# Performance work log

Hardware: AMD Instinct MI355X
Metric: run time of the kernel (lower is better)

The kernel has to match this reference:

```python
import jax, jax.numpy as jnp
import numpy as np

B, SQ, SV = 2, 2048, 2048
DV, DQ, DK, DO, H = 1024, 1280, 1024, 1024, 16
DHK, DHO = DK // H, DO // H


def setup_inputs() -> dict:
    key = jax.random.key(0)
    ks = jax.random.split(key, 8)
    pre_value_key = jax.random.normal(ks[0], (B, SV, DV), jnp.float32)
    pre_query = jax.random.normal(ks[1], (B, SQ, DQ), jnp.float32)
    value_key_masks = (jax.random.uniform(ks[2], (B, SV)) < 0.9).astype(jnp.float32)
    value_key_counts = jnp.maximum(value_key_masks.sum(-1), 1.0)
    s = 0.02
    Wq = jax.random.normal(ks[3], (DQ, DK), jnp.float32) * s
    bq = jnp.zeros((DK,), jnp.float32)
    Wk = jax.random.normal(ks[4], (DV, DK), jnp.float32) * s
    bk = jnp.zeros((DK,), jnp.float32)
    Wv = jax.random.normal(ks[5], (DV, DO), jnp.float32) * s
    bv = jnp.zeros((DO,), jnp.float32)
    overall_gain = jnp.ones((1, H, 1, 1), jnp.float32)
    overall_bias = jnp.full((1, H, 1, 1), -10.0, jnp.float32)
    return dict(pre_value_key=pre_value_key, pre_query=pre_query,
                value_key_masks=value_key_masks, value_key_counts=value_key_counts,
                Wq=Wq, bq=bq, Wk=Wk, bk=bk, Wv=Wv, bv=bv,
                overall_gain=overall_gain, overall_bias=overall_bias)


def _heads(x, h):
    # (B, S, D) -> (B, h, S, D//h)
    b, s, d = x.shape
    return x.reshape(b, s, h, d // h).transpose(0, 2, 1, 3)


def reference(pre_value_key, pre_query, value_key_masks, value_key_counts,
              Wq, bq, Wk, bk, Wv, bv, overall_gain, overall_bias):
    q = _heads(pre_query @ Wq + bq, H)        # (B,H,SQ,DHK)
    k = _heads(pre_value_key @ Wk + bk, H)    # (B,H,SV,DHK)
    v = _heads(pre_value_key @ Wv + bv, H)    # (B,H,SV,DHO)

    scores = jnp.einsum('bhqd,bhkd->bhqk', q, k) / jnp.sqrt(jnp.float32(DHK))

    mask = value_key_masks  # (B,SV), 0/1 float
    # pooled-score sigmoid gate (cross-attn branch)
    pooled = (scores * mask[:, None, None, :]).sum(-1, keepdims=True)
    pooled = pooled / value_key_counts[:, None, None, None]
    overall_weight = jax.nn.sigmoid(pooled * overall_gain + overall_bias)  # (B,H,SQ,1)

    add_mask = jnp.where(mask == 0, -jnp.inf, 0.0).astype(scores.dtype)
    sm = jax.nn.softmax(scores + add_mask[:, None, None, :], axis=-1)
    h = jnp.einsum('bhqk,bhkd->bhqd', sm, v)  # (B,H,SQ,DHO)

    pq_split = _heads(pre_query[:, :, :DO], H)  # (B,H,SQ,DHO)
    out = pq_split * (1.0 - overall_weight) + h * overall_weight
    out = out.transpose(0, 2, 1, 3).reshape(B, SQ, DO)
    out = jnp.concatenate([out, pre_query[:, :, DO:]], axis=-1)  # (B,SQ,DQ)
    return out
```

## Files before the change

### kernel.cpp

```cpp
#include <hip/hip_runtime.h>

typedef __attribute__((ext_vector_type(8))) __bf16 bf16x8;
typedef __attribute__((ext_vector_type(4))) float f32x4;
typedef __attribute__((ext_vector_type(16))) float f32x16;
typedef __attribute__((ext_vector_type(4))) unsigned short us4;
typedef __attribute__((ext_vector_type(4))) unsigned int u32x4;
typedef __attribute__((ext_vector_type(2))) unsigned int u32x2;
typedef __attribute__((address_space(3))) void* as3vp;
typedef const __attribute__((address_space(1))) void* as1vp;

#define GLOAD_LDS16(g, l) __builtin_amdgcn_global_load_lds((as1vp)(g), (as3vp)(l), 16, 0, 0)

#if __has_builtin(__builtin_amdgcn_exp2f)
#define EXP2(x) __builtin_amdgcn_exp2f(x)
#else
#define EXP2(x) __expf((x) * 0.6931471805599453f)
#endif

__device__ __forceinline__ unsigned short f2bf(float f) {
  unsigned u = __builtin_bit_cast(unsigned, f);
  u += 0x7FFFu + ((u >> 16) & 1u);
  return (unsigned short)(u >> 16);
}
__device__ __forceinline__ float bf2f(unsigned short u) {
  return __builtin_bit_cast(float, (unsigned)u << 16);
}
__device__ __forceinline__ unsigned int pkbf(float a, float b) {
  unsigned int r;
  asm("v_cvt_pk_bf16_f32 %0, %1, %2" : "=v"(r) : "v"(a), "v"(b));
  return r;
}

__global__ void cvt_pq_tail(const float* __restrict__ x, unsigned short* __restrict__ y,
                            float* __restrict__ out) {
  const int i = blockIdx.x * 256 + threadIdx.x;
  if (i >= 1310720) return;
  float4 v = ((const float4*)x)[i];
  us4 o;
  o.x = f2bf(v.x); o.y = f2bf(v.y); o.z = f2bf(v.z); o.w = f2bf(v.w);
  ((us4*)y)[i] = o;
  if ((i % 320) >= 256) ((float4*)out)[i] = v;
}

__global__ void cvt_f32_bf16(const float* __restrict__ x, unsigned short* __restrict__ y, int n4) {
  int i = blockIdx.x * 256 + threadIdx.x;
  if (i >= n4) return;
  float4 v = ((const float4*)x)[i];
  us4 o;
  o.x = f2bf(v.x); o.y = f2bf(v.y); o.z = f2bf(v.z); o.w = f2bf(v.w);
  ((us4*)y)[i] = o;
}

__global__ void transpose_w3(const float* __restrict__ Wq, const float* __restrict__ Wk,
                             const float* __restrict__ Wv,
                             unsigned short* __restrict__ WqT, unsigned short* __restrict__ WkT,
                             unsigned short* __restrict__ WvT) {
  const int z = blockIdx.z;
  const int K = (z == 0) ? 1280 : 1024;
  if ((int)blockIdx.y * 32 >= K) return;
  const float* W = (z == 0) ? Wq : ((z == 1) ? Wk : Wv);
  unsigned short* WT = (z == 0) ? WqT : ((z == 1) ? WkT : WvT);
  __shared__ float t[32][33];
  const int tx = threadIdx.x & 31, ty = threadIdx.x >> 5;
  const int n0 = blockIdx.x * 32, k0 = blockIdx.y * 32;
#pragma unroll
  for (int i = 0; i < 32; i += 8)
    t[ty + i][tx] = W[(size_t)(k0 + ty + i) * 1024 + n0 + tx];
  __syncthreads();
#pragma unroll
  for (int i = 0; i < 32; i += 8)
    WT[(size_t)(n0 + ty + i) * K + k0 + tx] = f2bf(t[tx][ty + i]);
}

__global__ void km_reduce(const unsigned short* __restrict__ Kbb, const float* __restrict__ mask,
                          float* __restrict__ km, float* __restrict__ addm) {
  if (blockIdx.x < 16) {
    const int i = blockIdx.x * 256 + threadIdx.x;
    addm[i] = (mask[i] != 0.f) ? 0.f : -1e30f;
  }
  __shared__ float red[16][64];
  const int bh = blockIdx.x >> 3, chunk = blockIdx.x & 7;
  const int b = bh >> 4;
  const int dg = (threadIdx.x & 15) * 4, rg = threadIdx.x >> 4;
  const unsigned short* kb = Kbb + (size_t)(b * 2048) * 1024 + (bh & 15) * 64 + dg;
  const float* mr = mask + b * 2048;
  float a0 = 0.f, a1 = 0.f, a2 = 0.f, a3 = 0.f;
  const int kv0 = chunk * 256;
#pragma unroll 4
  for (int kv = kv0 + rg; kv < kv0 + 256; kv += 16) {
    const float mv = mr[kv];
    us4 kq = *(const us4*)(kb + (size_t)kv * 1024);
    a0 = fmaf(mv, bf2f(kq.x), a0); a1 = fmaf(mv, bf2f(kq.y), a1);
    a2 = fmaf(mv, bf2f(kq.z), a2); a3 = fmaf(mv, bf2f(kq.w), a3);
  }
  red[rg][dg] = a0; red[rg][dg + 1] = a1; red[rg][dg + 2] = a2; red[rg][dg + 3] = a3;
  __syncthreads();
  if (threadIdx.x < 64) {
    float s = 0.f;
#pragma unroll
    for (int i = 0; i < 16; ++i) s += red[i][threadIdx.x];
    atomicAdd(&km[bh * 64 + threadIdx.x], s);
  }
}

__global__ __launch_bounds__(256, 2)
void gemm_all(const unsigned short* __restrict__ Aq,
              const unsigned short* __restrict__ Akv,
              const unsigned short* __restrict__ WqT,
              const unsigned short* __restrict__ WkT,
              const unsigned short* __restrict__ WvT,
              const float* __restrict__ bq,
              const float* __restrict__ bk,
              const float* __restrict__ bv,
              unsigned short* __restrict__ Qout,
              unsigned short* __restrict__ Kout,
              unsigned short* __restrict__ VFout) {
  __shared__ unsigned short sA[2][128 * 64];
  __shared__ unsigned short sB[2][128 * 64];
  const int z = blockIdx.z;
  const int KDIM = (z == 0) ? 1280 : 1024;
  const unsigned short* A = (z == 0) ? Aq : Akv;
  const unsigned short* Bt = (z == 0) ? WqT : ((z == 1) ? WkT : WvT);

  const int tid = threadIdx.x, lane = tid & 63, w = tid >> 6;
  const int l15 = lane & 15, lhi = lane >> 4;
  const int wm = w >> 1, wn = w & 1;
  const int row0 = blockIdx.x * 128, col0 = blockIdx.y * 128;

  const f32x4 zv = {0.f, 0.f, 0.f, 0.f};
  f32x4 acc[4][4];
#pragma unroll
  for (int m = 0; m < 4; ++m)
#pragma unroll
    for (int n = 0; n < 4; ++n) acc[m][n] = zv;

  auto stage = [&](int buf, int kt) {
#pragma unroll
    for (int i = 0; i < 4; ++i) {
      const int c = i * 256 + tid;
      const int r = c >> 3, kc = ((c & 7) ^ (r & 7)) * 8;
      GLOAD_LDS16(A + (size_t)(row0 + r) * KDIM + kt + kc, &sA[buf][0] + c * 8);
      GLOAD_LDS16(Bt + (size_t)(col0 + r) * KDIM + kt + kc, &sB[buf][0] + c * 8);
    }
  };

  const int NT = KDIM / 64;
  stage(0, 0);
  __syncthreads();
  int cur = 0;
  for (int t = 0; t < NT; ++t) {
    if (t + 1 < NT) stage(cur ^ 1, (t + 1) * 64);
    const unsigned short* sAb = &sA[cur][0];
    const unsigned short* sBb = &sB[cur][0];
#pragma unroll
    for (int ks = 0; ks < 2; ++ks) {
      const int koS = (ks * 32 + lhi * 8) ^ ((l15 & 7) * 8);
      bf16x8 af[4], bfr[4];
#pragma unroll
      for (int m = 0; m < 4; ++m) af[m] = *(const bf16x8*)(sAb + (wm * 64 + m * 16 + l15) * 64 + koS);
#pragma unroll
      for (int n = 0; n < 4; ++n) bfr[n] = *(const bf16x8*)(sBb + (wn * 64 + n * 16 + l15) * 64 + koS);
#pragma unroll
      for (int m = 0; m < 4; ++m)
#pragma unroll
        for (int n = 0; n < 4; ++n)
          acc[m][n] = __builtin_amdgcn_mfma_f32_16x16x32_bf16(af[m], bfr[n], acc[m][n], 0, 0, 0);
    }
    __syncthreads();
    cur ^= 1;
  }

  if (z <= 1) {
    unsigned short* C = (z == 0) ? Qout : Kout;
    const float* bias = (z == 0) ? bq : bk;
    const float scale = (z == 0) ? 0.18033688f : 1.0f;
#pragma unroll
    for (int n = 0; n < 4; ++n) {
      const int gc = col0 + wn * 64 + n * 16 + l15;
      const float bb = bias[gc];
#pragma unroll
      for (int m = 0; m < 4; ++m) {
        const int gr0 = row0 + wm * 64 + m * 16 + lhi * 4;
#pragma unroll
        for (int r = 0; r < 4; ++r)
          C[(size_t)(gr0 + r) * 1024 + gc] = f2bf((acc[m][n][r] + bb) * scale);
      }
    }
  } else {
    __syncthreads();
    unsigned* tb = (unsigned*)&sA[0][0];
#pragma unroll
    for (int n = 0; n < 4; ++n) {
      const int gcL = wn * 64 + n * 16 + l15;
      const float bb = bv[col0 + gcL];
#pragma unroll
      for (int m = 0; m < 4; ++m) {
#pragma unroll
        for (int k = 0; k < 2; ++k) {
          const int grPair = wm * 32 + m * 8 + lhi * 2 + k;
          const int W = (grPair & 3) | ((((grPair >> 2) ^ gcL) & 15) << 2);
          tb[gcL * 64 + W] = pkbf(acc[m][n][2 * k] + bb, acc[m][n][2 * k + 1] + bb);
        }
      }
    }
    __syncthreads();
    const int b_ = row0 >> 11;
#pragma unroll
    for (int it = 0; it < 8; ++it) {
      const int c = it * 256 + tid;
      const int gcL = (c & 63) + ((c >> 10) << 6);
      const int u = (c >> 6) & 15;
      const int W4 = (u ^ gcL) & 15;
      u32x4 o = *(const u32x4*)(tb + gcL * 64 + W4 * 4);
      const int kv0 = (row0 & 2047) + u * 8;
      const int ch = col0 + gcL;
      const int hh2 = ch >> 6, d = ch & 63;
      const int t2 = kv0 >> 6, ks2 = (kv0 >> 4) & 3, h5v = (kv0 >> 3) & 1;
      const size_t off = ((size_t)(b_ * 16 + hh2) << 17) +
                         (size_t)(((t2 * 4 + ks2) * 2 + (d >> 5)) * 64 + h5v * 32 + (d & 31)) * 8;
      *(u32x4*)(VFout + off) = o;
    }
  }
}

__global__ __launch_bounds__(256, 2)
void attn_fused(const unsigned short* __restrict__ Q,
                const unsigned short* __restrict__ Kb,
                const unsigned short* __restrict__ VF,
                const float* __restrict__ addm_g,
                const float* __restrict__ km,
                const float* __restrict__ counts,
                const float* __restrict__ gain,
                const float* __restrict__ gbias,
                const float* __restrict__ pq,
                float* __restrict__ out) {
  __shared__ __align__(16) char smem[32768];
  unsigned short* sK = (unsigned short*)smem;
  float* saddm = (float*)(smem + 16384);
  float* sOT = (float*)smem;

  const int tid = threadIdx.x, lane = tid & 63, w = tid >> 6;
  const int l31 = lane & 31, h5 = lane >> 5;
  const int f = blockIdx.x;
  const int qt = (f >> 3) & 15;
  const int bh = (f & 7) + 8 * (f >> 7);
  const int b = bh >> 4, hh = bh & 15;
  const int q0 = qt * 128;

  GLOAD_LDS16(addm_g + b * 2048 + tid * 4, (char*)saddm + tid * 16);
  GLOAD_LDS16(addm_g + b * 2048 + 1024 + tid * 4, (char*)saddm + 4096 + tid * 16);

  bf16x8 qf[4];
  {
    const unsigned short* qp = Q + (size_t)(b * 2048 + q0 + w * 32 + l31) * 1024 + hh * 64 + h5 * 8;
#pragma unroll
    for (int ks = 0; ks < 4; ++ks) qf[ks] = *(const bf16x8*)(qp + ks * 16);
  }

  float pl_s = 0.f;
  {
    const float* kmp = km + (b * 16 + hh) * 64 + h5 * 8;
#pragma unroll
    for (int ks = 0; ks < 4; ++ks) {
      f32x4 ka = *(const f32x4*)(kmp + ks * 16);
      f32x4 kb4 = *(const f32x4*)(kmp + ks * 16 + 4);
#pragma unroll
      for (int j = 0; j < 4; ++j)
        pl_s += (float)qf[ks][j] * ka[j] + (float)qf[ks][j + 4] * kb4[j];
    }
    float ta = pl_s, tb = pl_s;
    asm("v_permlane32_swap_b32 %0, %1" : "+v"(ta), "+v"(tb));
    pl_s = ta + tb;
  }

  const unsigned short* Kbase = Kb + (size_t)(b * 2048) * 1024 + hh * 64;
  const unsigned short* VFb = VF + ((size_t)bh << 17) + lane * 8;

  f32x16 o0, o1, l_vec;
#pragma unroll
  for (int r = 0; r < 16; ++r) { o0[r] = 0.f; o1[r] = 0.f; l_vec[r] = 0.f; }
  float m_ = -1e30f;

  auto stageK = [&](int buf, int kv) {
#pragma unroll
    for (int i = 0; i < 2; ++i) {
      const int c = i * 256 + tid;
      const int r = c >> 3, sl = (c & 7) ^ (r & 7);
      GLOAD_LDS16(Kbase + (size_t)(kv + r) * 1024 + sl * 8, (char*)sK + buf * 8192 + c * 16);
    }
  };

  bf16x8 vf[8];
  auto ldV = [&](int t) {
    const unsigned short* p = VFb + (size_t)t * 4096;
#pragma unroll
    for (int i = 0; i < 8; ++i) vf[i] = *(const bf16x8*)(p + i * 512);
  };

  stageK(0, 0);
  __syncthreads();
  int cur = 0;

  for (int t = 0; t < 32; ++t) {
    if (t < 31) stageK(cur ^ 1, (t + 1) * 64);
    ldV(t);
    const char* sKc = (const char*)sK + cur * 8192;

    f32x16 s0, s1;
#pragma unroll
    for (int g = 0; g < 4; ++g) {
      f32x4 a0 = *(const f32x4*)(saddm + t * 64 + g * 8 + h5 * 4);
      f32x4 a1 = *(const f32x4*)(saddm + t * 64 + 32 + g * 8 + h5 * 4);
#pragma unroll
      for (int j = 0; j < 4; ++j) { s0[g * 4 + j] = a0[j]; s1[g * 4 + j] = a1[j]; }
    }

#pragma unroll
    for (int ks = 0; ks < 4; ++ks) {
      const int sl = (((ks * 2 + h5) ^ (l31 & 7)) * 16);
      bf16x8 k0 = *(const bf16x8*)(sKc + l31 * 128 + sl);
      bf16x8 k1 = *(const bf16x8*)(sKc + (32 + l31) * 128 + sl);
      s0 = __builtin_amdgcn_mfma_f32_32x32x16_bf16(k0, qf[ks], s0, 0, 0, 0);
      s1 = __builtin_amdgcn_mfma_f32_32x32x16_bf16(k1, qf[ks], s1, 0, 0, 0);
    }

    f32x16 mx;
#pragma unroll
    for (int r = 0; r < 16; ++r) mx[r] = fmaxf(s0[r], s1[r]);
    float t8[8];
#pragma unroll
    for (int r = 0; r < 8; ++r) t8[r] = fmaxf(mx[r], mx[r + 8]);
    float tp = fmaxf(fmaxf(fmaxf(t8[0], t8[1]), fmaxf(t8[2], t8[3])),
                     fmaxf(fmaxf(t8[4], t8[5]), fmaxf(t8[6], t8[7])));
    {
      float ta = tp, tb = tp;
      asm("v_permlane32_swap_b32 %0, %1" : "+v"(ta), "+v"(tb));
      tp = fmaxf(ta, tb);
    }
    if (__any(tp > m_ + 11.0f)) {
      const float mnew = fmaxf(m_, tp);
      const float corr = EXP2(m_ - mnew);
      m_ = mnew;
      l_vec *= corr; o0 *= corr; o1 *= corr;
    }

    f32x16 p0, p1;
#pragma unroll
    for (int r = 0; r < 16; ++r) p0[r] = EXP2(s0[r] - m_);
#pragma unroll
    for (int r = 0; r < 16; ++r) p1[r] = EXP2(s1[r] - m_);
    l_vec += p0; l_vec += p1;

    bf16x8 pfs[4];
    {
      unsigned x0 = pkbf(p0[0], p0[1]), y0 = pkbf(p0[2], p0[3]);
      unsigned z0 = pkbf(p0[4], p0[5]), w0 = pkbf(p0[6], p0[7]);
      asm("v_permlane32_swap_b32 %0, %1" : "+v"(x0), "+v"(z0));
      asm("v_permlane32_swap_b32 %0, %1" : "+v"(y0), "+v"(w0));
      u32x4 f0 = {x0, y0, z0, w0};
      pfs[0] = __builtin_bit_cast(bf16x8, f0);
      unsigned x1 = pkbf(p0[8], p0[9]), y1 = pkbf(p0[10], p0[11]);
      unsigned z1 = pkbf(p0[12], p0[13]), w1 = pkbf(p0[14], p0[15]);
      asm("v_permlane32_swap_b32 %0, %1" : "+v"(x1), "+v"(z1));
      asm("v_permlane32_swap_b32 %0, %1" : "+v"(y1), "+v"(w1));
      u32x4 f1 = {x1, y1, z1, w1};
      pfs[1] = __builtin_bit_cast(bf16x8, f1);
      unsigned x2 = pkbf(p1[0], p1[1]), y2 = pkbf(p1[2], p1[3]);
      unsigned z2 = pkbf(p1[4], p1[5]), w2 = pkbf(p1[6], p1[7]);
      asm("v_permlane32_swap_b32 %0, %1" : "+v"(x2), "+v"(z2));
      asm("v_permlane32_swap_b32 %0, %1" : "+v"(y2), "+v"(w2));
      u32x4 f2 = {x2, y2, z2, w2};
      pfs[2] = __builtin_bit_cast(bf16x8, f2);
      unsigned x3 = pkbf(p1[8], p1[9]), y3 = pkbf(p1[10], p1[11]);
      unsigned z3 = pkbf(p1[12], p1[13]), w3 = pkbf(p1[14], p1[15]);
      asm("v_permlane32_swap_b32 %0, %1" : "+v"(x3), "+v"(z3));
      asm("v_permlane32_swap_b32 %0, %1" : "+v"(y3), "+v"(w3));
      u32x4 f3 = {x3, y3, z3, w3};
      pfs[3] = __builtin_bit_cast(bf16x8, f3);
    }

#pragma unroll
    for (int ks = 0; ks < 4; ++ks) {
      o0 = __builtin_amdgcn_mfma_f32_32x32x16_bf16(vf[ks * 2], pfs[ks], o0, 0, 0, 0);
      o1 = __builtin_amdgcn_mfma_f32_32x32x16_bf16(vf[ks * 2 + 1], pfs[ks], o1, 0, 0, 0);
    }
    __syncthreads();
    cur ^= 1;
  }

  float l_s;
  {
    float a[8];
#pragma unroll
    for (int r = 0; r < 8; ++r) a[r] = l_vec[r] + l_vec[r + 8];
    l_s = ((a[0] + a[1]) + (a[2] + a[3])) + ((a[4] + a[5]) + (a[6] + a[7]));
    float ta = l_s, tb = l_s;
    asm("v_permlane32_swap_b32 %0, %1" : "+v"(ta), "+v"(tb));
    l_s = ta + tb;
  }
  const float po = pl_s * 0.6931471805599453f / counts[b];
  const float wgv = 1.f / (1.f + __expf(-(po * gain[hh] + gbias[hh])));
  const float invl = 1.f / l_s;

  __syncthreads();
  float* myOT = sOT + w * 2048;
#pragma unroll
  for (int r = 0; r < 16; ++r) {
    const int d0 = (r & 3) + 8 * (r >> 2) + 4 * h5;
    myOT[d0 * 32 + (l31 ^ (d0 & 31))] = o0[r] * invl;
    const int d1 = d0 + 32;
    myOT[d1 * 32 + (l31 ^ (d1 & 31))] = o1[r] * invl;
  }
  __syncthreads();
  const size_t rowbase = (size_t)(b * 2048 + q0 + w * 32) * 1280 + hh * 64 + lane;
  const float* pqrow = pq + rowbase;
  float* outrow = out + rowbase;
#pragma unroll 4
  for (int i = 0; i < 32; ++i) {
    const float hval = myOT[lane * 32 + (i ^ (lane & 31))];
    const float wgrow = __shfl(wgv, i, 64);
    const float pv = pqrow[(size_t)i * 1280];
    outrow[(size_t)i * 1280] = fmaf(hval - pv, wgrow, pv);
  }
}

extern "C" void kernel_launch(void* const* d_in, const int* in_sizes, int n_in,
                              void* d_out, int out_size, void* d_ws, size_t ws_size,
                              hipStream_t stream) {
  const float* pre_vk = (const float*)d_in[0];
  const float* pre_q  = (const float*)d_in[1];
  const float* vmask  = (const float*)d_in[2];
  const float* vcnt   = (const float*)d_in[3];
  const float* Wq = (const float*)d_in[4];
  const float* bq = (const float*)d_in[5];
  const float* Wk = (const float*)d_in[6];
  const float* bk = (const float*)d_in[7];
  const float* Wv = (const float*)d_in[8];
  const float* bv = (const float*)d_in[9];
  const float* gain  = (const float*)d_in[10];
  const float* gbias = (const float*)d_in[11];
  float* out = (float*)d_out;

  char* ws = (char*)d_ws;
  unsigned short* pq_bf = (unsigned short*)(ws);
  unsigned short* pv_bf = (unsigned short*)(ws + 10485760);
  unsigned short* WqT   = (unsigned short*)(ws + 18874368);
  unsigned short* WkT   = (unsigned short*)(ws + 21495808);
  unsigned short* WvT   = (unsigned short*)(ws + 23592960);
  unsigned short* Qb    = (unsigned short*)(ws + 25690112);
  unsigned short* Kbb   = (unsigned short*)(ws + 34078720);
  unsigned short* VFb   = (unsigned short*)(ws + 42467328);
  float*          kmb   = (float*)(ws + 50855936);
  float*          addm  = (float*)(ws + 50864128);

  hipMemsetAsync(kmb, 0, 2 * 16 * 64 * sizeof(float), stream);
  cvt_pq_tail<<<5120, 256, 0, stream>>>(pre_q, pq_bf, out);
  cvt_f32_bf16<<<4096, 256, 0, stream>>>(pre_vk, pv_bf, 1048576);
  transpose_w3<<<dim3(32, 40, 3), 256, 0, stream>>>(Wq, Wk, Wv, WqT, WkT, WvT);
  gemm_all<<<dim3(32, 8, 3), 256, 0, stream>>>(pq_bf, pv_bf, WqT, WkT, WvT, bq, bk, bv, Qb, Kbb, VFb);
  km_reduce<<<256, 256, 0, stream>>>(Kbb, vmask, kmb, addm);
  attn_fused<<<512, 256, 0, stream>>>(Qb, Kbb, VFb, addm, kmb, vcnt, gain, gbias, pre_q, out);
}
```

Before: 121.3 us.

## Merge prep kernels into one launch and halve GEMM K-tile for occupancy

```diff
diff --git a/kernel.cpp b/kernel.cpp
--- a/kernel.cpp
+++ b/kernel.cpp
@@ -5,7 +5,6 @@
 typedef __attribute__((ext_vector_type(16))) float f32x16;
 typedef __attribute__((ext_vector_type(4))) unsigned short us4;
 typedef __attribute__((ext_vector_type(4))) unsigned int u32x4;
-typedef __attribute__((ext_vector_type(2))) unsigned int u32x2;
 typedef __attribute__((address_space(3))) void* as3vp;
 typedef const __attribute__((address_space(1))) void* as1vp;
 
@@ -31,45 +30,45 @@
   return r;
 }
 
-__global__ void cvt_pq_tail(const float* __restrict__ x, unsigned short* __restrict__ y,
-                            float* __restrict__ out) {
-  const int i = blockIdx.x * 256 + threadIdx.x;
-  if (i >= 1310720) return;
-  float4 v = ((const float4*)x)[i];
-  us4 o;
-  o.x = f2bf(v.x); o.y = f2bf(v.y); o.z = f2bf(v.z); o.w = f2bf(v.w);
-  ((us4*)y)[i] = o;
-  if ((i % 320) >= 256) ((float4*)out)[i] = v;
-}
-
-__global__ void cvt_f32_bf16(const float* __restrict__ x, unsigned short* __restrict__ y, int n4) {
-  int i = blockIdx.x * 256 + threadIdx.x;
-  if (i >= n4) return;
-  float4 v = ((const float4*)x)[i];
-  us4 o;
-  o.x = f2bf(v.x); o.y = f2bf(v.y); o.z = f2bf(v.z); o.w = f2bf(v.w);
-  ((us4*)y)[i] = o;
-}
-
-__global__ void transpose_w3(const float* __restrict__ Wq, const float* __restrict__ Wk,
-                             const float* __restrict__ Wv,
-                             unsigned short* __restrict__ WqT, unsigned short* __restrict__ WkT,
-                             unsigned short* __restrict__ WvT) {
-  const int z = blockIdx.z;
-  const int K = (z == 0) ? 1280 : 1024;
-  if ((int)blockIdx.y * 32 >= K) return;
-  const float* W = (z == 0) ? Wq : ((z == 1) ? Wk : Wv);
-  unsigned short* WT = (z == 0) ? WqT : ((z == 1) ? WkT : WvT);
-  __shared__ float t[32][33];
-  const int tx = threadIdx.x & 31, ty = threadIdx.x >> 5;
-  const int n0 = blockIdx.x * 32, k0 = blockIdx.y * 32;
-#pragma unroll
-  for (int i = 0; i < 32; i += 8)
-    t[ty + i][tx] = W[(size_t)(k0 + ty + i) * 1024 + n0 + tx];
-  __syncthreads();
-#pragma unroll
-  for (int i = 0; i < 32; i += 8)
-    WT[(size_t)(n0 + ty + i) * K + k0 + tx] = f2bf(t[tx][ty + i]);
+__global__ void prep_all(const float* __restrict__ pre_q, const float* __restrict__ pre_vk,
+                         const float* __restrict__ Wq, const float* __restrict__ Wk,
+                         const float* __restrict__ Wv,
+                         unsigned short* __restrict__ pq_bf, unsigned short* __restrict__ pv_bf,
+                         unsigned short* __restrict__ WqT, unsigned short* __restrict__ WkT,
+                         unsigned short* __restrict__ WvT, float* __restrict__ out) {
+  __shared__ float tsh[32][33];
+  const int bid = blockIdx.x, tid = threadIdx.x;
+  if (bid < 5120) {
+    const int i = bid * 256 + tid;
+    float4 v = ((const float4*)pre_q)[i];
+    us4 o;
+    o.x = f2bf(v.x); o.y = f2bf(v.y); o.z = f2bf(v.z); o.w = f2bf(v.w);
+    ((us4*)pq_bf)[i] = o;
+    if ((i % 320) >= 256) ((float4*)out)[i] = v;
+  } else if (bid < 9216) {
+    const int i = (bid - 5120) * 256 + tid;
+    float4 v = ((const float4*)pre_vk)[i];
+    us4 o;
+    o.x = f2bf(v.x); o.y = f2bf(v.y); o.z = f2bf(v.z); o.w = f2bf(v.w);
+    ((us4*)pv_bf)[i] = o;
+  } else {
+    const int tb = bid - 9216;
+    const int z = tb / 1280, rem = tb % 1280;
+    const int x = rem & 31, y = rem >> 5;
+    const int K = (z == 0) ? 1280 : 1024;
+    if (y * 32 >= K) return;
+    const float* W = (z == 0) ? Wq : ((z == 1) ? Wk : Wv);
+    unsigned short* WT = (z == 0) ? WqT : ((z == 1) ? WkT : WvT);
+    const int tx = tid & 31, ty = tid >> 5;
+    const int n0 = x * 32, k0 = y * 32;
+#pragma unroll
+    for (int i = 0; i < 32; i += 8)
+      tsh[ty + i][tx] = W[(size_t)(k0 + ty + i) * 1024 + n0 + tx];
+    __syncthreads();
+#pragma unroll
+    for (int i = 0; i < 32; i += 8)
+      WT[(size_t)(n0 + ty + i) * K + k0 + tx] = f2bf(tsh[tx][ty + i]);
+  }
 }
 
 __global__ void km_reduce(const unsigned short* __restrict__ Kbb, const float* __restrict__ mask,
@@ -103,7 +102,7 @@
   }
 }
 
-__global__ __launch_bounds__(256, 2)
+__global__ __launch_bounds__(256, 3)
 void gemm_all(const unsigned short* __restrict__ Aq,
               const unsigned short* __restrict__ Akv,
               const unsigned short* __restrict__ WqT,
@@ -115,8 +114,7 @@
               unsigned short* __restrict__ Qout,
               unsigned short* __restrict__ Kout,
               unsigned short* __restrict__ VFout) {
-  __shared__ unsigned short sA[2][128 * 64];
-  __shared__ unsigned short sB[2][128 * 64];
+  __shared__ unsigned short sAB[2][2][128 * 32];
   const int z = blockIdx.z;
   const int KDIM = (z == 0) ? 1280 : 1024;
   const unsigned short* A = (z == 0) ? Aq : Akv;
@@ -136,36 +134,33 @@
 
   auto stage = [&](int buf, int kt) {
 #pragma unroll
-    for (int i = 0; i < 4; ++i) {
+    for (int i = 0; i < 2; ++i) {
       const int c = i * 256 + tid;
-      const int r = c >> 3, kc = ((c & 7) ^ (r & 7)) * 8;
-      GLOAD_LDS16(A + (size_t)(row0 + r) * KDIM + kt + kc, &sA[buf][0] + c * 8);
-      GLOAD_LDS16(Bt + (size_t)(col0 + r) * KDIM + kt + kc, &sB[buf][0] + c * 8);
+      const int r = c >> 2, kc = ((c & 3) ^ (r & 3)) * 8;
+      GLOAD_LDS16(A + (size_t)(row0 + r) * KDIM + kt + kc, &sAB[buf][0][0] + c * 8);
+      GLOAD_LDS16(Bt + (size_t)(col0 + r) * KDIM + kt + kc, &sAB[buf][1][0] + c * 8);
     }
   };
 
-  const int NT = KDIM / 64;
+  const int NT = KDIM / 32;
   stage(0, 0);
   __syncthreads();
   int cur = 0;
   for (int t = 0; t < NT; ++t) {
-    if (t + 1 < NT) stage(cur ^ 1, (t + 1) * 64);
-    const unsigned short* sAb = &sA[cur][0];
-    const unsigned short* sBb = &sB[cur][0];
-#pragma unroll
-    for (int ks = 0; ks < 2; ++ks) {
-      const int koS = (ks * 32 + lhi * 8) ^ ((l15 & 7) * 8);
-      bf16x8 af[4], bfr[4];
-#pragma unroll
-      for (int m = 0; m < 4; ++m) af[m] = *(const bf16x8*)(sAb + (wm * 64 + m * 16 + l15) * 64 + koS);
-#pragma unroll
-      for (int n = 0; n < 4; ++n) bfr[n] = *(const bf16x8*)(sBb + (wn * 64 + n * 16 + l15) * 64 + koS);
-#pragma unroll
-      for (int m = 0; m < 4; ++m)
-#pragma unroll
-        for (int n = 0; n < 4; ++n)
-          acc[m][n] = __builtin_amdgcn_mfma_f32_16x16x32_bf16(af[m], bfr[n], acc[m][n], 0, 0, 0);
-    }
+    if (t + 1 < NT) stage(cur ^ 1, (t + 1) * 32);
+    const unsigned short* sAb = &sAB[cur][0][0];
+    const unsigned short* sBb = &sAB[cur][1][0];
+    const int koS = ((lhi ^ (l15 & 3)) * 8);
+    bf16x8 af[4], bfr[4];
+#pragma unroll
+    for (int m = 0; m < 4; ++m) af[m] = *(const bf16x8*)(sAb + (wm * 64 + m * 16 + l15) * 32 + koS);
+#pragma unroll
+    for (int n = 0; n < 4; ++n) bfr[n] = *(const bf16x8*)(sBb + (wn * 64 + n * 16 + l15) * 32 + koS);
+#pragma unroll
+    for (int m = 0; m < 4; ++m)
+#pragma unroll
+      for (int n = 0; n < 4; ++n)
+        acc[m][n] = __builtin_amdgcn_mfma_f32_16x16x32_bf16(af[m], bfr[n], acc[m][n], 0, 0, 0);
     __syncthreads();
     cur ^= 1;
   }
@@ -188,7 +183,7 @@
     }
   } else {
     __syncthreads();
-    unsigned* tb = (unsigned*)&sA[0][0];
+    unsigned* tb = (unsigned*)&sAB[0][0][0];
 #pragma unroll
     for (int n = 0; n < 4; ++n) {
       const int gcL = wn * 64 + n * 16 + l15;
@@ -454,9 +449,8 @@
   float*          addm  = (float*)(ws + 50864128);
 
   hipMemsetAsync(kmb, 0, 2 * 16 * 64 * sizeof(float), stream);
-  cvt_pq_tail<<<5120, 256, 0, stream>>>(pre_q, pq_bf, out);
-  cvt_f32_bf16<<<4096, 256, 0, stream>>>(pre_vk, pv_bf, 1048576);
-  transpose_w3<<<dim3(32, 40, 3), 256, 0, stream>>>(Wq, Wk, Wv, WqT, WkT, WvT);
+  prep_all<<<13056, 256, 0, stream>>>(pre_q, pre_vk, Wq, Wk, Wv,
+                                      pq_bf, pv_bf, WqT, WkT, WvT, out);
   gemm_all<<<dim3(32, 8, 3), 256, 0, stream>>>(pq_bf, pv_bf, WqT, WkT, WvT, bq, bk, bv, Qb, Kbb, VFb);
   km_reduce<<<256, 256, 0, stream>>>(Kbb, vmask, kmb, addm);
   attn_fused<<<512, 256, 0, stream>>>(Qb, Kbb, VFb, addm, kmb, vcnt, gain, gbias, pre_q, out);
```

Result: faster. 115.0 us (-5.2%).
